# Kernel optimization log

Hardware: AMD Instinct MI355X
Metric: run time of the kernel (lower is better)

Reference implementation:

```python
import jax, jax.numpy as jnp
import numpy as np

B = 131072
N_STEPS = 216
H = 1.0 / 216.0            # Euler step size
A_Z0 = 0.005               # baseline wander amplitude (mV)
F2 = 0.25                  # baseline wander frequency (Hz)
OMEGA = 2.0 * np.pi        # angular velocity (rrpc = 1 s RR interval)
X0 = -0.417750770388669
Y0 = -0.9085616622823985
MIN_VAL = -0.01563
MAX_VAL = 0.042557


def setup_inputs() -> dict:
    key = jax.random.key(0)
    k1, k2 = jax.random.split(key)
    x = jax.random.uniform(k1, (B, 15), dtype=jnp.float32)   # [a,b,theta] x 5 waves, interleaved
    v0 = jax.random.normal(k2, (B,), dtype=jnp.float32) * 0.01
    return {"x": x, "v0": v0}


def _euler_integrate(params, v0):
    # params: [B,15] interleaved (a_i, b_i, theta_i) for P,Q,R,S,T waves
    a = params[:, 0::3]      # [B,5]
    b = params[:, 1::3]      # [B,5]
    theta = params[:, 2::3]  # [B,5]
    bsz = params.shape[0]
    dt = params.dtype
    x0 = jnp.full((bsz,), X0, dtype=dt)
    y0 = jnp.full((bsz,), Y0, dtype=dt)

    def step(carry, t):
        x, y, z = carry
        alpha = 1.0 - jnp.sqrt(x * x + y * y)
        f_x = alpha * x - OMEGA * y
        f_y = alpha * y + OMEGA * x
        th = jnp.arctan2(y, x)                      # [B]
        dth = jnp.fmod(th[:, None] - theta, 2.0 * np.pi)  # [B,5]
        gauss = a * dth * jnp.exp(-(dth * dth) / (2.0 * b * b))
        z0_t = A_Z0 * jnp.sin(2.0 * np.pi * F2 * t)
        f_z = -jnp.sum(gauss, axis=1) - (z - z0_t)
        x_n = x + H * f_x
        y_n = y + H * f_y
        z_n = z + H * f_z
        return (x_n, y_n, z_n), z_n

    ts = jnp.arange(N_STEPS, dtype=dt) / 216.0      # t=0 for step 0, then +1/216 each step
    _, z_t = jax.lax.scan(step, (x0, y0, v0.astype(dt)), ts)
    return z_t.T                                    # [B,216]


def _scale_signal(z):
    zmin = jnp.min(z, axis=1, keepdims=True)
    zmax = jnp.max(z, axis=1, keepdims=True)
    return (z - zmin) * MAX_VAL / (zmax - zmin) + MIN_VAL


def reference(x, v0):
    z = _euler_integrate(x, v0)
    return _scale_signal(z)
```

## Files before the change

### kernel.cpp

```cpp
#include <hip/hip_runtime.h>
#include <math.h>

#define NSTEPS 216
#define BLK 64
#define CT 54
#define CSTR 55

__device__ float g_th[NSTEPS];
__device__ float g_hz0[NSTEPS];

__global__ void traj_kernel() {
    __shared__ float xs[NSTEPS], ys[NSTEPS];
    const int t = threadIdx.x;
    if (t == 0) {
        float x = (float)(-0.417750770388669);
        float y = (float)(-0.9085616622823985);
        const float W = (float)(2.0 * M_PI);
        const float H = (float)(1.0 / 216.0);
        for (int n = 0; n < NSTEPS; ++n) {
            xs[n] = x;
            ys[n] = y;
            float alpha = 1.0f - sqrtf(x * x + y * y);
            float fx = alpha * x - W * y;
            float fy = alpha * y + W * x;
            x = x + H * fx;
            y = y + H * fy;
        }
    }
    __syncthreads();
    if (t < NSTEPS) {
        g_th[t] = atan2f(ys[t], xs[t]);
        float tf = (float)t / 216.0f;
        g_hz0[t] = (float)(1.0 / 216.0) * (0.005f * sinf(1.5707964f * tf));
    }
}

__global__ __launch_bounds__(BLK) void euler_kernel(const float* __restrict__ prm,
                                                    const float* __restrict__ v0,
                                                    float* __restrict__ out) {
    __shared__ float th_s[NSTEPS];
    __shared__ float hz0_s[NSTEPS];
    __shared__ float st_s[BLK * CSTR];

    const int tid = threadIdx.x;
    for (int i = tid; i < NSTEPS; i += BLK) {
        th_s[i] = g_th[i];
        hz0_s[i] = g_hz0[i];
    }

    const int b = blockIdx.x * BLK + tid;
    const float* p = prm + (size_t)b * 15;

    float tj[5], cj[5], la[5];
#pragma unroll
    for (int j = 0; j < 5; ++j) {
        float a  = p[3 * j + 0];
        float bb = p[3 * j + 1];
        tj[j] = p[3 * j + 2];
        cj[j] = -1.0f / (2.0f * bb * bb);
        la[j] = __logf(a);
    }

    const float zinit = v0[b];
    const float H = (float)(1.0 / 216.0);
    const float K = 1.0f - H;

    __syncthreads();

    float z = zinit;
    float zmin = 3.4e38f, zmax = -3.4e38f;
#pragma unroll 4
    for (int t = 0; t < NSTEPS; ++t) {
        float th = th_s[t];
        float G = 0.0f;
#pragma unroll
        for (int j = 0; j < 5; ++j) {
            float d = th - tj[j];
            G = fmaf(d, __expf(fmaf(d * d, cj[j], la[j])), G);
        }
        z = fmaf(z, K, fmaf(-H, G, hz0_s[t]));
        zmin = fminf(zmin, z);
        zmax = fmaxf(zmax, z);
    }
    const float s = 0.042557f / (zmax - zmin);
    const float o = fmaf(-zmin, s, -0.01563f);

    z = zinit;
    float* outB = out + (size_t)blockIdx.x * (BLK * NSTEPS);
    for (int c0 = 0; c0 < NSTEPS; c0 += CT) {
#pragma unroll 4
        for (int tc = 0; tc < CT; ++tc) {
            int t = c0 + tc;
            float th = th_s[t];
            float G = 0.0f;
#pragma unroll
            for (int j = 0; j < 5; ++j) {
                float d = th - tj[j];
                G = fmaf(d, __expf(fmaf(d * d, cj[j], la[j])), G);
            }
            z = fmaf(z, K, fmaf(-H, G, hz0_s[t]));
            st_s[tid * CSTR + tc] = fmaf(z, s, o);
        }
        __syncthreads();
#pragma unroll 6
        for (int k = 0; k < CT; ++k) {
            unsigned idx = (unsigned)tid + BLK * k;
            unsigned r = idx / 54u;
            unsigned tt = idx - r * 54u;
            outB[r * NSTEPS + c0 + tt] = st_s[r * CSTR + tt];
        }
        __syncthreads();
    }
}

extern "C" void kernel_launch(void* const* d_in, const int* in_sizes, int n_in,
                              void* d_out, int out_size, void* d_ws, size_t ws_size,
                              hipStream_t stream) {
    const float* x  = (const float*)d_in[0];
    const float* v0 = (const float*)d_in[1];
    float* out = (float*)d_out;
    const int nb = in_sizes[1];

    hipLaunchKernelGGL(traj_kernel, dim3(1), dim3(256), 0, stream);
    hipLaunchKernelGGL(euler_kernel, dim3(nb / BLK), dim3(BLK), 0, stream, x, v0, out);
}
```

Measured before the change: 191.7 us.

## Parallelize Euler recurrence over time with wave-wide prefix scan per row

The linear z recurrence is rewritten as a scaled prefix sum using precomputed powers of K and their inverses, so each row is handled by one 64-lane wave and each lane owns 4 time steps. This removes the serial 216-step loop that was run twice, along with the shared-memory transpose staging. Each lane now writes its four outputs with one coalesced float4 store. The cost is wave shuffles for the scan and the min/max reductions, a 4x larger table, and possible float rounding drift from the K^-n factors growing to about e.

Result: no change. 195.4 us (+1.9%).

```diff
diff --git a/kernel.cpp b/kernel.cpp
--- a/kernel.cpp
+++ b/kernel.cpp
@@ -2,55 +2,50 @@
 #include <math.h>
 
 #define NSTEPS 216
-#define BLK 64
-#define CT 54
-#define CSTR 55
+#define RPB 4
+#define BLK 256
 
-__device__ float g_th[NSTEPS];
-__device__ float g_hz0[NSTEPS];
+__device__ float4 g_tbl[NSTEPS];
 
 __global__ void traj_kernel() {
-    __shared__ float xs[NSTEPS], ys[NSTEPS];
+    __shared__ float xs[NSTEPS], ys[NSTEPS], kps[NSTEPS], kis[NSTEPS];
     const int t = threadIdx.x;
     if (t == 0) {
         float x = (float)(-0.417750770388669);
         float y = (float)(-0.9085616622823985);
         const float W = (float)(2.0 * M_PI);
-        const float H = (float)(1.0 / 216.0);
+        const float H = 1.0f / 216.0f;
+        const double Kd = (double)(1.0f - H);
+        const double Kid = 1.0 / Kd;
+        double kp = 1.0, ki = 1.0;
         for (int n = 0; n < NSTEPS; ++n) {
-            xs[n] = x;
-            ys[n] = y;
+            xs[n] = x;  ys[n] = y;
+            kps[n] = (float)kp;  kis[n] = (float)ki;
             float alpha = 1.0f - sqrtf(x * x + y * y);
             float fx = alpha * x - W * y;
             float fy = alpha * y + W * x;
             x = x + H * fx;
             y = y + H * fy;
+            kp *= Kd;  ki *= Kid;
         }
     }
     __syncthreads();
     if (t < NSTEPS) {
-        g_th[t] = atan2f(ys[t], xs[t]);
+        float th = atan2f(ys[t], xs[t]);
         float tf = (float)t / 216.0f;
-        g_hz0[t] = (float)(1.0 / 216.0) * (0.005f * sinf(1.5707964f * tf));
+        float hz0 = (1.0f / 216.0f) * (0.005f * sinf(1.5707964f * tf));
+        g_tbl[t] = make_float4(th, hz0, kis[t], kps[t]);
     }
 }
 
 __global__ __launch_bounds__(BLK) void euler_kernel(const float* __restrict__ prm,
                                                     const float* __restrict__ v0,
                                                     float* __restrict__ out) {
-    __shared__ float th_s[NSTEPS];
-    __shared__ float hz0_s[NSTEPS];
-    __shared__ float st_s[BLK * CSTR];
+    const int lane = threadIdx.x & 63;
+    const int wav  = threadIdx.x >> 6;
+    const int row  = blockIdx.x * RPB + wav;
 
-    const int tid = threadIdx.x;
-    for (int i = tid; i < NSTEPS; i += BLK) {
-        th_s[i] = g_th[i];
-        hz0_s[i] = g_hz0[i];
-    }
-
-    const int b = blockIdx.x * BLK + tid;
-    const float* p = prm + (size_t)b * 15;
-
+    const float* p = prm + (size_t)row * 15;
     float tj[5], cj[5], la[5];
 #pragma unroll
     for (int j = 0; j < 5; ++j) {
@@ -60,56 +55,61 @@
         cj[j] = -1.0f / (2.0f * bb * bb);
         la[j] = __logf(a);
     }
-
-    const float zinit = v0[b];
-    const float H = (float)(1.0 / 216.0);
+    const float z0v = v0[row];
+    const float H = 1.0f / 216.0f;
     const float K = 1.0f - H;
 
-    __syncthreads();
+    int sb = lane * 4;
+    if (sb > NSTEPS - 4) sb = NSTEPS - 4;
 
-    float z = zinit;
-    float zmin = 3.4e38f, zmax = -3.4e38f;
-#pragma unroll 4
-    for (int t = 0; t < NSTEPS; ++t) {
-        float th = th_s[t];
+    float loc[4], zK[4];
+    float run = 0.0f;
+#pragma unroll
+    for (int q = 0; q < 4; ++q) {
+        float4 e = g_tbl[sb + q];
+        float th = e.x;
         float G = 0.0f;
 #pragma unroll
         for (int j = 0; j < 5; ++j) {
             float d = th - tj[j];
             G = fmaf(d, __expf(fmaf(d * d, cj[j], la[j])), G);
         }
-        z = fmaf(z, K, fmaf(-H, G, hz0_s[t]));
-        zmin = fminf(zmin, z);
-        zmax = fmaxf(zmax, z);
+        float u = fmaf(-H, G, e.y);
+        run += e.z * u;
+        loc[q] = run;
+        zK[q] = e.w;
+    }
+
+    float scan = run;
+#pragma unroll
+    for (int d = 1; d < 64; d <<= 1) {
+        float o = __shfl_up(scan, (unsigned)d, 64);
+        if (lane >= d) scan += o;
+    }
+    const float excl = scan - run;
+
+    const float Kz0 = K * z0v;
+    float z[4];
+    float zmin = 3.4e38f, zmax = -3.4e38f;
+#pragma unroll
+    for (int q = 0; q < 4; ++q) {
+        z[q] = zK[q] * (Kz0 + (excl + loc[q]));
+        zmin = fminf(zmin, z[q]);
+        zmax = fmaxf(zmax, z[q]);
+    }
+    if (lane >= 54) { zmin = 3.4e38f; zmax = -3.4e38f; }
+#pragma unroll
+    for (int d = 1; d < 64; d <<= 1) {
+        zmin = fminf(zmin, __shfl_xor(zmin, d, 64));
+        zmax = fmaxf(zmax, __shfl_xor(zmax, d, 64));
     }
     const float s = 0.042557f / (zmax - zmin);
     const float o = fmaf(-zmin, s, -0.01563f);
 
-    z = zinit;
-    float* outB = out + (size_t)blockIdx.x * (BLK * NSTEPS);
-    for (int c0 = 0; c0 < NSTEPS; c0 += CT) {
-#pragma unroll 4
-        for (int tc = 0; tc < CT; ++tc) {
-            int t = c0 + tc;
-            float th = th_s[t];
-            float G = 0.0f;
-#pragma unroll
-            for (int j = 0; j < 5; ++j) {
-                float d = th - tj[j];
-                G = fmaf(d, __expf(fmaf(d * d, cj[j], la[j])), G);
-            }
-            z = fmaf(z, K, fmaf(-H, G, hz0_s[t]));
-            st_s[tid * CSTR + tc] = fmaf(z, s, o);
-        }
-        __syncthreads();
-#pragma unroll 6
-        for (int k = 0; k < CT; ++k) {
-            unsigned idx = (unsigned)tid + BLK * k;
-            unsigned r = idx / 54u;
-            unsigned tt = idx - r * 54u;
-            outB[r * NSTEPS + c0 + tt] = st_s[r * CSTR + tt];
-        }
-        __syncthreads();
+    if (lane < 54) {
+        float4 v = { fmaf(z[0], s, o), fmaf(z[1], s, o),
+                     fmaf(z[2], s, o), fmaf(z[3], s, o) };
+        *(float4*)(out + (size_t)row * NSTEPS + lane * 4) = v;
     }
 }
 
@@ -122,5 +122,5 @@
     const int nb = in_sizes[1];
 
     hipLaunchKernelGGL(traj_kernel, dim3(1), dim3(256), 0, stream);
-    hipLaunchKernelGGL(euler_kernel, dim3(nb / BLK), dim3(BLK), 0, stream, x, v0, out);
+    hipLaunchKernelGGL(euler_kernel, dim3(nb / RPB), dim3(BLK), 0, stream, x, v0, out);
 }
```
